# Performance work log

Hardware: AMD Instinct MI355X
Metric: run time of the kernel (lower is better)

## Reference

```python
import jax, jax.numpy as jnp
import numpy as np

NUM_HEADS = 8
WINDOW = 5
DILATION = 1


def _offsets(window, dilation):
    r = dilation * (window // 2)
    return [(dy, dx) for dy in range(-r, r + 1, dilation)
            for dx in range(-r, r + 1, dilation)]


def _neighbors(x, window, dilation):
    # x: [B, heads, head_dim, Hc, Wc] -> [B, heads, K, head_dim, Hc, Wc]
    B, Hn, hd, Hc, Wc = x.shape
    r = dilation * (window // 2)
    xp = jnp.pad(x, ((0, 0), (0, 0), (0, 0), (r, r), (r, r)))
    offs = _offsets(window, dilation)
    return jnp.stack(
        [xp[..., r + dy:r + dy + Hc, r + dx:r + dx + Wc] for dy, dx in offs],
        axis=2)


def _valid_mask(Hc, Wc, window, dilation):
    # [K, Hc, Wc] bool: True where the shifted neighbor lies inside the map
    ys = jnp.arange(Hc)
    xs = jnp.arange(Wc)
    offs = _offsets(window, dilation)
    return jnp.stack(
        [(((ys + dy) >= 0) & ((ys + dy) < Hc))[:, None]
         & (((xs + dx) >= 0) & ((xs + dx) < Wc))[None, :]
         for dy, dx in offs], axis=0)


def _align_to_query_grid(t, out_h, out_w, scale):
    # repeat coarse lattice onto the fine query grid via anchor indexing
    y = jnp.clip(jnp.arange(out_h) // scale, 0, t.shape[-2] - 1)
    x = jnp.clip(jnp.arange(out_w) // scale, 0, t.shape[-1] - 1)
    return jnp.take(jnp.take(t, y, axis=-2), x, axis=-1)


def setup_inputs() -> dict:
    key = jax.random.key(0)
    k1, k2 = jax.random.split(key)
    k = jax.random.normal(k1, (2, 128, 48, 48), dtype=jnp.float32)
    v = jax.random.normal(k2, (2, 128, 48, 48), dtype=jnp.float32)
    return {"k": k, "v": v, "query_height": 96, "query_width": 96,
            "scale_factor": 2}


def reference(k, v, query_height, query_width, scale_factor):
    B, C, Hc, Wc = k.shape
    hd = C // NUM_HEADS
    kh = k.reshape(B, NUM_HEADS, hd, Hc, Wc)
    vh = v.reshape(B, NUM_HEADS, hd, Hc, Wc)
    k_nb = _neighbors(kh, WINDOW, DILATION)  # [B,H,K,hd,Hc,Wc]
    v_nb = _neighbors(vh, WINDOW, DILATION)
    mask = _valid_mask(Hc, Wc, WINDOW, DILATION)  # [K,Hc,Wc]
    K = mask.shape[0]
    mask = jnp.broadcast_to(mask[None, None], (B, NUM_HEADS, K, Hc, Wc))
    k_nb = _align_to_query_grid(k_nb, query_height, query_width, scale_factor)
    v_nb = _align_to_query_grid(v_nb, query_height, query_width, scale_factor)
    mask = _align_to_query_grid(mask, query_height, query_width, scale_factor)
    return (k_nb, v_nb, mask)
```

## Files before the change

### kernel.cpp

```cpp
#include <hip/hip_runtime.h>


#define KV_ELEMS  58982400LL
#define MASK_OFF  117964800LL

__global__ __launch_bounds__(256) void kv_expand_kernel(
    const float* __restrict__ k, const float* __restrict__ v,
    float* __restrict__ out_k, float* __restrict__ out_v) {
    int tid = blockIdx.x * blockDim.x + threadIdx.x;
    int x4 = tid % 24;  int t = tid / 24;
    int y  = t % 96;    t /= 96;
    int d  = t % 16;    t /= 16;
    int kk = t % 25;    t /= 25;
    int h  = t % 8;
    int b  = t / 8;

    int dy = kk / 5 - 2;
    int dx = kk % 5 - 2;
    int yy = (y >> 1) + dy;
    bool vy = (unsigned)yy < 48u;
    int xc0 = 2 * x4 + dx;
    int xc1 = xc0 + 1;
    bool v0 = vy && ((unsigned)xc0 < 48u);
    bool v1 = vy && ((unsigned)xc1 < 48u);

    int base = ((b * 128 + h * 16 + d) * 48 + (vy ? yy : 0)) * 48;
    float k0 = v0 ? k[base + xc0] : 0.0f;
    float k1 = v1 ? k[base + xc1] : 0.0f;
    float w0 = v0 ? v[base + xc0] : 0.0f;
    float w1 = v1 ? v[base + xc1] : 0.0f;

    float4 ok = make_float4(k0, k0, k1, k1);
    float4 ov = make_float4(w0, w0, w1, w1);
    reinterpret_cast<float4*>(out_k)[tid] = ok;
    reinterpret_cast<float4*>(out_v)[tid] = ov;
}

__global__ __launch_bounds__(256) void mask_kernel(float* __restrict__ out_m) {
    int tid = blockIdx.x * blockDim.x + threadIdx.x;
    int x4 = tid % 24;  int t = tid / 24;
    int y  = t % 96;    t /= 96;
    int kk = t % 25;

    int dy = kk / 5 - 2;
    int dx = kk % 5 - 2;
    int yy = (y >> 1) + dy;
    bool vy = (unsigned)yy < 48u;
    int xc0 = 2 * x4 + dx;
    bool v0 = vy && ((unsigned)xc0 < 48u);
    bool v1 = vy && ((unsigned)(xc0 + 1) < 48u);

    float m0 = v0 ? 1.0f : 0.0f;
    float m1 = v1 ? 1.0f : 0.0f;
    reinterpret_cast<float4*>(out_m)[tid] = make_float4(m0, m0, m1, m1);
}

extern "C" void kernel_launch(void* const* d_in, const int* in_sizes, int n_in,
                              void* d_out, int out_size, void* d_ws, size_t ws_size,
                              hipStream_t stream) {
    const float* k = (const float*)d_in[0];
    const float* v = (const float*)d_in[1];
    float* out = (float*)d_out;
    float* out_k = out;
    float* out_v = out + KV_ELEMS;
    float* out_m = out + MASK_OFF;

    kv_expand_kernel<<<57600, 256, 0, stream>>>(k, v, out_k, out_v);
    mask_kernel<<<3600, 256, 0, stream>>>(out_m);
}
```

Before: 478.7 us.

## Fuse KV expand and mask kernels; reuse loaded values for duplicated rows

Merges the KV expansion and mask kernels into one launch on a 2D grid, where blockIdx.y selects the (batch-head, offset, channel) plane or a mask plane. Each thread now loads one coarse row element and writes it to both fine rows (y and y+1), halving the loads and the index math per output. Index decomposition becomes cheaper through shifts and a smaller modulo chain. The kernel is still write-bandwidth bound, so the gain depends on how much instruction and launch overhead was limiting throughput.

```diff
diff --git a/kernel.cpp b/kernel.cpp
--- a/kernel.cpp
+++ b/kernel.cpp
@@ -1,58 +1,68 @@
 #include <hip/hip_runtime.h>
 
 
-#define KV_ELEMS  58982400LL
-#define MASK_OFF  117964800LL
+#define HC 48
+#define WC 48
 
-__global__ __launch_bounds__(256) void kv_expand_kernel(
+__global__ __launch_bounds__(384) void fused_expand(
     const float* __restrict__ k, const float* __restrict__ v,
-    float* __restrict__ out_k, float* __restrict__ out_v) {
-    int tid = blockIdx.x * blockDim.x + threadIdx.x;
-    int x4 = tid % 24;  int t = tid / 24;
-    int y  = t % 96;    t /= 96;
-    int d  = t % 16;    t /= 16;
-    int kk = t % 25;    t /= 25;
-    int h  = t % 8;
-    int b  = t / 8;
+    float* __restrict__ out_k, float* __restrict__ out_v,
+    float* __restrict__ out_m) {
+    int t  = blockIdx.x * 384 + threadIdx.x;
+    int yc = t / 24;
+    int x4 = t - yc * 24;
+    int by = blockIdx.y;
 
-    int dy = kk / 5 - 2;
-    int dx = kk % 5 - 2;
-    int yy = (y >> 1) + dy;
-    bool vy = (unsigned)yy < 48u;
-    int xc0 = 2 * x4 + dx;
-    int xc1 = xc0 + 1;
-    bool v0 = vy && ((unsigned)xc0 < 48u);
-    bool v1 = vy && ((unsigned)xc1 < 48u);
+    if (by < 6400) {
+        int d    = by & 15;
+        int rest = by >> 4;
+        int kk   = rest % 25;
+        int bh   = rest / 25;
+        int dy = kk / 5 - 2;
+        int dx = kk % 5 - 2;
 
-    int base = ((b * 128 + h * 16 + d) * 48 + (vy ? yy : 0)) * 48;
-    float k0 = v0 ? k[base + xc0] : 0.0f;
-    float k1 = v1 ? k[base + xc1] : 0.0f;
-    float w0 = v0 ? v[base + xc0] : 0.0f;
-    float w1 = v1 ? v[base + xc1] : 0.0f;
+        int yy  = yc + dy;
+        bool vy = (unsigned)yy < (unsigned)HC;
+        int xc0 = 2 * x4 + dx;
+        int xc1 = xc0 + 1;
+        bool m0 = vy && ((unsigned)xc0 < (unsigned)WC);
+        bool m1 = vy && ((unsigned)xc1 < (unsigned)WC);
 
-    float4 ok = make_float4(k0, k0, k1, k1);
-    float4 ov = make_float4(w0, w0, w1, w1);
-    reinterpret_cast<float4*>(out_k)[tid] = ok;
-    reinterpret_cast<float4*>(out_v)[tid] = ov;
-}
+        int src = ((bh * 16 + d) * HC + (vy ? yy : 0)) * WC;
+        float k0 = m0 ? k[src + xc0] : 0.0f;
+        float k1 = m1 ? k[src + xc1] : 0.0f;
+        float w0 = m0 ? v[src + xc0] : 0.0f;
+        float w1 = m1 ? v[src + xc1] : 0.0f;
 
-__global__ __launch_bounds__(256) void mask_kernel(float* __restrict__ out_m) {
-    int tid = blockIdx.x * blockDim.x + threadIdx.x;
-    int x4 = tid % 24;  int t = tid / 24;
-    int y  = t % 96;    t /= 96;
-    int kk = t % 25;
+        float4 ok = make_float4(k0, k0, k1, k1);
+        float4 ov = make_float4(w0, w0, w1, w1);
+        int o = by * 2304 + yc * 48 + x4;
+        float4* pk = reinterpret_cast<float4*>(out_k);
+        float4* pv = reinterpret_cast<float4*>(out_v);
+        pk[o]      = ok;
+        pk[o + 24] = ok;
+        pv[o]      = ov;
+        pv[o + 24] = ov;
+    } else {
+        int q  = by - 6400;
+        int kk = q % 25;
+        int dy = kk / 5 - 2;
+        int dx = kk % 5 - 2;
 
-    int dy = kk / 5 - 2;
-    int dx = kk % 5 - 2;
-    int yy = (y >> 1) + dy;
-    bool vy = (unsigned)yy < 48u;
-    int xc0 = 2 * x4 + dx;
-    bool v0 = vy && ((unsigned)xc0 < 48u);
-    bool v1 = vy && ((unsigned)(xc0 + 1) < 48u);
+        int yy  = yc + dy;
+        bool vy = (unsigned)yy < (unsigned)HC;
+        int xc0 = 2 * x4 + dx;
+        bool m0 = vy && ((unsigned)xc0 < (unsigned)WC);
+        bool m1 = vy && ((unsigned)(xc0 + 1) < (unsigned)WC);
 
-    float m0 = v0 ? 1.0f : 0.0f;
-    float m1 = v1 ? 1.0f : 0.0f;
-    reinterpret_cast<float4*>(out_m)[tid] = make_float4(m0, m0, m1, m1);
+        float f0 = m0 ? 1.0f : 0.0f;
+        float f1 = m1 ? 1.0f : 0.0f;
+        float4 m = make_float4(f0, f0, f1, f1);
+        int o = q * 2304 + yc * 48 + x4;
+        float4* pm = reinterpret_cast<float4*>(out_m);
+        pm[o]      = m;
+        pm[o + 24] = m;
+    }
 }
 
 extern "C" void kernel_launch(void* const* d_in, const int* in_sizes, int n_in,
@@ -60,11 +70,11 @@
                               hipStream_t stream) {
     const float* k = (const float*)d_in[0];
     const float* v = (const float*)d_in[1];
-    float* out = (float*)d_out;
+    float* out   = (float*)d_out;
     float* out_k = out;
-    float* out_v = out + KV_ELEMS;
-    float* out_m = out + MASK_OFF;
+    float* out_v = out + 58982400;
+    float* out_m = out + 117964800;
 
-    kv_expand_kernel<<<57600, 256, 0, stream>>>(k, v, out_k, out_v);
-    mask_kernel<<<3600, 256, 0, stream>>>(out_m);
+    dim3 grid(3, 6800, 1);
+    fused_expand<<<grid, 384, 0, stream>>>(k, v, out_k, out_v, out_m);
 }
```

Result: no change. 486.6 us (+1.7%).
